# Optimization experiments

Hardware: AMD Instinct MI355X
Metric: run time of the kernel (lower is better)

## Reference

```python
import jax, jax.numpy as jnp
import numpy as np

L_F, HOP, DELTA, L_S, COND, GH = 32, 16, 3, 96, 32, 64
B, T = 128, 48000


def setup_inputs() -> dict:
    key = jax.random.key(0)
    ks = jax.random.split(key, 12)
    s = 0.05
    return {
        "x": jax.random.normal(ks[0], (B, T), jnp.float32),
        # GRU (PyTorch layout): weight_ih (3H, L_S), weight_hh (3H, H)
        "W_ih": jax.random.normal(ks[1], (3 * GH, L_S), jnp.float32) * s,
        "W_hh": jax.random.normal(ks[2], (3 * GH, GH), jnp.float32) * s,
        "b_ih": jax.random.normal(ks[3], (3 * GH,), jnp.float32) * s,
        "b_hh": jax.random.normal(ks[4], (3 * GH,), jnp.float32) * s,
        # SlowBranch output projection -> cond_dim
        "W_cs": jax.random.normal(ks[5], (COND, GH), jnp.float32) * s,
        "b_cs": jax.random.normal(ks[6], (COND,), jnp.float32) * s,
        # FastEC MLP
        "W1": jax.random.normal(ks[7], (GH, L_F + COND), jnp.float32) * s,
        "b1": jax.random.normal(ks[8], (GH,), jnp.float32) * s,
        "W2": jax.random.normal(ks[9], (L_F, GH), jnp.float32) * s,
        "b2": jax.random.normal(ks[10], (L_F,), jnp.float32) * s,
    }


def reference(x, W_ih, W_hh, b_ih, b_hh, W_cs, b_cs, W1, b1, W2, b2):
    Bsz, Tlen = x.shape
    Nf = (Tlen - L_F) // HOP + 1
    win_s = DELTA * HOP * 2
    hop_s = DELTA * HOP
    Ns = (Tlen - win_s) // hop_s + 1

    f_starts = jnp.arange(Nf) * HOP                      # (Nf,)
    fast_idx = f_starts[:, None] + jnp.arange(L_F)       # (Nf, L_F)
    fast_frames = x[:, fast_idx]                         # (B, Nf, L_F)

    s_starts = jnp.arange(Ns) * hop_s
    slow_frames = x[:, s_starts[:, None] + jnp.arange(win_s)]  # (B, Ns, L_S)

    # Single-layer GRU over slow frames (PyTorch gate order r, z, n)
    def step(h, xt):
        gi = xt @ W_ih.T + b_ih                          # (B, 3H)
        gh = h @ W_hh.T + b_hh
        i_r, i_z, i_n = jnp.split(gi, 3, axis=-1)
        h_r, h_z, h_n = jnp.split(gh, 3, axis=-1)
        r = jax.nn.sigmoid(i_r + h_r)
        z = jax.nn.sigmoid(i_z + h_z)
        n = jnp.tanh(i_n + r * h_n)
        hn = (1.0 - z) * n + z * h
        return hn, hn

    h0 = jnp.zeros((Bsz, GH), x.dtype)
    _, hs = jax.lax.scan(step, h0, jnp.swapaxes(slow_frames, 0, 1))
    hs = jnp.swapaxes(hs, 0, 1)                          # (B, Ns, GH)
    c_s = hs @ W_cs.T + b_cs                             # (B, Ns, COND)

    # per-fast-frame conditioning vector (gather)
    idx = jnp.clip(jnp.arange(Nf) // DELTA - 1, 0, None)
    c = c_s[:, idx]                                      # (B, Nf, COND)

    # FastEC batched over all frames at once
    h = jnp.concatenate([fast_frames, c], axis=-1)       # (B, Nf, L_F+COND)
    h = jax.nn.relu(h @ W1.T + b1)
    y = h @ W2.T + b2                                    # (B, Nf, L_F)

    # overlap-add scatter
    out = jnp.zeros_like(x).at[:, fast_idx].add(y)
    return out
```

## Files before the change

kernel.cpp:

```cpp
#include <hip/hip_runtime.h>

constexpr int Bn  = 128;
constexpr int Tn  = 48000;
constexpr int NFn = 2999;
constexpr int NSn = 999;
constexpr int G3n = 192;
constexpr int GHn = 64;

typedef float f2 __attribute__((ext_vector_type(2)));
typedef float f4 __attribute__((ext_vector_type(4)));

__global__ __launch_bounds__(192) void gi_kernel(const float* __restrict__ x,
                                                 const float* __restrict__ W_ih,
                                                 const float* __restrict__ b_ih,
                                                 float* __restrict__ GI) {
  __shared__ __align__(16) float WT[48 * 196];
  __shared__ __align__(16) float xs[1584];
  const int tile = blockIdx.x;
  const int b    = blockIdx.y;
  const int t0   = tile * 32;
  const int nt   = min(32, NSn - t0);
  const int tid  = threadIdx.x;

  const int span = (nt - 1) * 48 + 96;
  for (int i = tid; i < 1584; i += 192)
    xs[i] = (i < span) ? x[(size_t)b * Tn + t0 * 48 + i] : 0.0f;

  const int jq = tid % 48;
  const int tg = tid / 48;
  const int j0 = jq * 4;

  float acc[8][4];
#pragma unroll
  for (int u = 0; u < 8; ++u)
#pragma unroll
    for (int jj = 0; jj < 4; ++jj) acc[u][jj] = b_ih[j0 + jj];

  for (int half = 0; half < 2; ++half) {
    __syncthreads();
    for (int e = tid; e < 192 * 48; e += 192) {
      int j = e / 48, k = e % 48;
      WT[k * 196 + j] = W_ih[j * 96 + half * 48 + k];
    }
    __syncthreads();
    for (int kc = 0; kc < 48; kc += 4) {
      f4 wq[4];
#pragma unroll
      for (int kk = 0; kk < 4; ++kk)
        wq[kk] = *(const f4*)&WT[(kc + kk) * 196 + j0];
      f4 xq[8];
#pragma unroll
      for (int u = 0; u < 8; ++u)
        xq[u] = *(const f4*)&xs[(tg * 8 + u) * 48 + half * 48 + kc];
#pragma unroll
      for (int u = 0; u < 8; ++u) {
#pragma unroll
        for (int kk = 0; kk < 4; ++kk) {
          const float xv = xq[u][kk];
          acc[u][0] = fmaf(xv, wq[kk][0], acc[u][0]);
          acc[u][1] = fmaf(xv, wq[kk][1], acc[u][1]);
          acc[u][2] = fmaf(xv, wq[kk][2], acc[u][2]);
          acc[u][3] = fmaf(xv, wq[kk][3], acc[u][3]);
        }
      }
    }
  }

#pragma unroll
  for (int u = 0; u < 8; ++u) {
    int tl = tg * 8 + u;
    if (tl < nt) {
      float4 st = make_float4(acc[u][0], acc[u][1], acc[u][2], acc[u][3]);
      *(float4*)&GI[(size_t)(b * NSn + t0 + tl) * G3n + j0] = st;
    }
  }
}

__device__ __forceinline__ float fsigmoid(float v) {
  return __fdividef(1.0f, 1.0f + __expf(-v));
}
__device__ __forceinline__ float ftanh_f(float v) {
  return 1.0f - __fdividef(2.0f, __expf(2.0f * v) + 1.0f);
}

__device__ __forceinline__ void gru_body(const float* __restrict__ GI,
                                         const float* __restrict__ W_hh,
                                         const float* __restrict__ b_hh,
                                         float* __restrict__ hs,
                                         float* hbuf, int b, int j) {
  f2 wr2[32], wz2[32], wn2[32];
  const f2* Wr = (const f2*)(W_hh + (size_t)j * 64);
  const f2* Wz = (const f2*)(W_hh + (size_t)(j + 64) * 64);
  const f2* Wn = (const f2*)(W_hh + (size_t)(j + 128) * 64);
#pragma unroll
  for (int q = 0; q < 32; ++q) { wr2[q] = Wr[q]; wz2[q] = Wz[q]; wn2[q] = Wn[q]; }
#pragma unroll
  for (int q = 0; q < 32; ++q) {
    asm volatile("" : "+v"(wr2[q]));
    asm volatile("" : "+v"(wz2[q]));
    asm volatile("" : "+v"(wn2[q]));
  }
  const float br = b_hh[j], bz = b_hh[j + 64], bn = b_hh[j + 128];

  hbuf[j] = 0.0f;
  float hj = 0.0f;
  __builtin_amdgcn_wave_barrier();

  const float* gp = GI + (size_t)b * NSn * G3n;
  float* hsp = hs + (size_t)b * NSn * GHn;

  float pr0, pr1, pr2, pz0, pz1, pz2, pn0, pn1, pn2;
  pr0 = gp[0 * G3n + j];       pz0 = gp[0 * G3n + 64 + j];  pn0 = gp[0 * G3n + 128 + j];
  pr1 = gp[1 * G3n + j];       pz1 = gp[1 * G3n + 64 + j];  pn1 = gp[1 * G3n + 128 + j];

  for (int t = 0; t < NSn; ++t) {
    const size_t off = (size_t)min(t + 2, NSn - 1) * G3n;
    pr2 = gp[off + j];
    pz2 = gp[off + 64 + j];
    pn2 = gp[off + 128 + j];

    const f2* h2 = (const f2*)hbuf;
    f2 ar0 = {0.f, 0.f}, ar1 = {0.f, 0.f}, ar2 = {0.f, 0.f}, ar3 = {0.f, 0.f};
    f2 az0 = {0.f, 0.f}, az1 = {0.f, 0.f}, az2 = {0.f, 0.f}, az3 = {0.f, 0.f};
    f2 an0 = {0.f, 0.f}, an1 = {0.f, 0.f}, an2 = {0.f, 0.f}, an3 = {0.f, 0.f};
#pragma unroll
    for (int q = 0; q < 8; ++q) {
      f2 h0 = h2[q * 4 + 0], h1 = h2[q * 4 + 1], h2v = h2[q * 4 + 2], h3 = h2[q * 4 + 3];
      ar0 += wr2[q * 4 + 0] * h0; ar1 += wr2[q * 4 + 1] * h1;
      ar2 += wr2[q * 4 + 2] * h2v; ar3 += wr2[q * 4 + 3] * h3;
      az0 += wz2[q * 4 + 0] * h0; az1 += wz2[q * 4 + 1] * h1;
      az2 += wz2[q * 4 + 2] * h2v; az3 += wz2[q * 4 + 3] * h3;
      an0 += wn2[q * 4 + 0] * h0; an1 += wn2[q * 4 + 1] * h1;
      an2 += wn2[q * 4 + 2] * h2v; an3 += wn2[q * 4 + 3] * h3;
    }
    f2 sr = (ar0 + ar1) + (ar2 + ar3);
    f2 sz = (az0 + az1) + (az2 + az3);
    f2 sn = (an0 + an1) + (an2 + an3);

    float r = fsigmoid(pr0 + br + sr.x + sr.y);
    float z = fsigmoid(pz0 + bz + sz.x + sz.y);
    float n = ftanh_f(fmaf(r, bn + sn.x + sn.y, pn0));
    float hn = fmaf(z, hj - n, n);

    __builtin_amdgcn_wave_barrier();
    hbuf[j] = hn;
    __builtin_amdgcn_wave_barrier();
    hj = hn;
    hsp[(size_t)t * GHn + j] = hn;

    pr0 = pr1; pr1 = pr2;
    pz0 = pz1; pz1 = pz2;
    pn0 = pn1; pn1 = pn2;
  }
}

__global__ __attribute__((amdgpu_flat_work_group_size(64, 64),
                          amdgpu_waves_per_eu(1, 1),
                          amdgpu_num_vgpr(256)))
void gru_kernel(const float* __restrict__ GI,
                const float* __restrict__ W_hh,
                const float* __restrict__ b_hh,
                float* __restrict__ hs) {
  __shared__ __align__(16) float hbuf[64];
  gru_body(GI, W_hh, b_hh, hs, hbuf, blockIdx.x, threadIdx.x);
}

constexpr int UCHUNK = 125;
constexpr int NCH    = 24;

__global__ __attribute__((amdgpu_flat_work_group_size(64, 64),
                          amdgpu_waves_per_eu(1, 1),
                          amdgpu_num_vgpr(256)))
void fat_kernel(const float* __restrict__ GI,
                const float* __restrict__ W_hh,
                const float* __restrict__ b_hh,
                float* __restrict__ hs,
                const float* __restrict__ x,
                const float* __restrict__ W1,
                const float* __restrict__ b1,
                float* __restrict__ U) {
  __shared__ __align__(16) float hbuf[64];
  __shared__ __align__(16) float xs[UCHUNK * 16 + 16];
  const int tid = threadIdx.x;

  if (blockIdx.x < Bn) {
    __builtin_amdgcn_s_setprio(1);
    gru_body(GI, W_hh, b_hh, hs, hbuf, blockIdx.x, tid);
    __builtin_amdgcn_s_setprio(0);
    return;
  }

  const int ub = blockIdx.x - Bn;
  const int b  = ub / NCH;
  const int ch = ub % NCH;
  const int fA = ch * UCHUNK;
  const int fE = min(fA + UCHUNK, NFn);
  const int o  = tid;

  const int nsamp = (fE - fA - 1) * 16 + 32;
  for (int i = tid; i < nsamp; i += 64)
    xs[i] = x[(size_t)b * Tn + fA * 16 + i];

  f4 w1f[8];
#pragma unroll
  for (int i = 0; i < 8; ++i)
    w1f[i] = *(const f4*)&W1[(size_t)o * 64 + 4 * i];
  const float bo = b1[o];
  __syncthreads();

  float* Up = U + ((size_t)b * NFn) * GHn + o;
  for (int f = fA; f < fE; ++f) {
    const f4* xq = (const f4*)&xs[(f - fA) * 16];
    float a0 = bo, a1 = 0.f, a2 = 0.f, a3 = 0.f;
#pragma unroll
    for (int i = 0; i < 8; ++i) {
      f4 xv = xq[i];
      a0 = fmaf(xv[0], w1f[i][0], a0);
      a1 = fmaf(xv[1], w1f[i][1], a1);
      a2 = fmaf(xv[2], w1f[i][2], a2);
      a3 = fmaf(xv[3], w1f[i][3], a3);
    }
    Up[(size_t)f * GHn] = (a0 + a1) + (a2 + a3);
  }
}

__global__ __launch_bounds__(256) void d_kernel(const float* __restrict__ hs,
                                                const float* __restrict__ W_cs,
                                                const float* __restrict__ b_cs,
                                                const float* __restrict__ W1,
                                                float* __restrict__ d) {
  __shared__ __align__(16) float WcT[64 * 36];
  __shared__ __align__(16) float W1cT[32 * 68];
  __shared__ __align__(16) float hsl[32 * 65];
  __shared__ __align__(16) float cloc[32 * 36];
  __shared__ __align__(16) float bcs[32];
  const int tile = blockIdx.x;
  const int b    = blockIdx.y;
  const int t0   = tile * 32;
  const int nt   = min(32, NSn - t0);
  const int tid  = threadIdx.x;

  for (int e = tid; e < 32 * 64; e += 256) {
    int i = e >> 6, k = e & 63;
    WcT[k * 36 + i] = W_cs[e];
  }
  for (int e = tid; e < 64 * 32; e += 256) {
    int o = e >> 5, i = e & 31;
    W1cT[i * 68 + o] = W1[(size_t)o * 64 + 32 + i];
  }
  for (int e = tid; e < nt * 64; e += 256) {
    int t = e >> 6, k = e & 63;
    hsl[t * 65 + k] = hs[((size_t)b * NSn + t0 + t) * GHn + k];
  }
  if (tid < 32) bcs[tid] = b_cs[tid];
  __syncthreads();

  {
    const int iq = tid & 7;
    const int t  = tid >> 3;
    if (t < nt) {
      float4 acc = *(const float4*)&bcs[iq * 4];
      const float* hr = &hsl[t * 65];
#pragma unroll 4
      for (int k = 0; k < 64; ++k) {
        float hv = hr[k];
        float4 w = *(const float4*)&WcT[k * 36 + iq * 4];
        acc.x = fmaf(w.x, hv, acc.x);
        acc.y = fmaf(w.y, hv, acc.y);
        acc.z = fmaf(w.z, hv, acc.z);
        acc.w = fmaf(w.w, hv, acc.w);
      }
      *(float4*)&cloc[t * 36 + iq * 4] = acc;
    }
  }
  __syncthreads();

  for (int it = tid; it < 32 * 16; it += 256) {
    const int oq = it & 15;
    const int t  = it >> 4;
    if (t < nt) {
      float a0 = 0.f, a1 = 0.f, a2 = 0.f, a3 = 0.f;
      const float* cr = &cloc[t * 36];
#pragma unroll 4
      for (int i = 0; i < 32; ++i) {
        float cv = cr[i];
        float4 w = *(const float4*)&W1cT[i * 68 + oq * 4];
        a0 = fmaf(w.x, cv, a0);
        a1 = fmaf(w.y, cv, a1);
        a2 = fmaf(w.z, cv, a2);
        a3 = fmaf(w.w, cv, a3);
      }
      float4 st = make_float4(a0, a1, a2, a3);
      *(float4*)&d[((size_t)b * NSn + t0 + t) * GHn + oq * 4] = st;
    }
  }
}

__global__ __launch_bounds__(256) void cs_kernel(const float* __restrict__ hs,
                                                 const float* __restrict__ W_cs,
                                                 const float* __restrict__ b_cs,
                                                 float* __restrict__ cs) {
  __shared__ __align__(16) float WcT[64 * 36];
  __shared__ __align__(16) float hsl[32 * 65];
  __shared__ __align__(16) float bcs[32];
  const int tile = blockIdx.x;
  const int b    = blockIdx.y;
  const int t0   = tile * 32;
  const int nt   = min(32, NSn - t0);
  const int tid  = threadIdx.x;

  for (int e = tid; e < 32 * 64; e += 256) {
    int i = e >> 6, k = e & 63;
    WcT[k * 36 + i] = W_cs[e];
  }
  for (int e = tid; e < nt * 64; e += 256) {
    int t = e >> 6, k = e & 63;
    hsl[t * 65 + k] = hs[((size_t)b * NSn + t0 + t) * GHn + k];
  }
  if (tid < 32) bcs[tid] = b_cs[tid];
  __syncthreads();

  const int oq = tid & 7;
  const int t  = tid >> 3;
  if (t < nt) {
    float4 acc = *(const float4*)&bcs[oq * 4];
    const float* hr = &hsl[t * 65];
#pragma unroll 4
    for (int k = 0; k < 64; ++k) {
      float hv = hr[k];
      float4 w = *(const float4*)&WcT[k * 36 + oq * 4];
      acc.x = fmaf(w.x, hv, acc.x);
      acc.y = fmaf(w.y, hv, acc.y);
      acc.z = fmaf(w.z, hv, acc.z);
      acc.w = fmaf(w.w, hv, acc.w);
    }
    *(float4*)&cs[((size_t)b * NSn + t0 + t) * 32 + oq * 4] = acc;
  }
}

__global__ __launch_bounds__(256) void out2_kernel(const float* __restrict__ U,
                                                   const float* __restrict__ d,
                                                   const float* __restrict__ W2,
                                                   const float* __restrict__ b2,
                                                   float* __restrict__ out) {
  __shared__ __align__(16) float h1loc[33 * 68];
  __shared__ __align__(16) float W2T[64 * 36];
  __shared__ __align__(16) float yloc[33 * 32];
  __shared__ __align__(16) float dloc[12][68];
  __shared__ __align__(16) float bb2[32];

  const int fb  = blockIdx.x;
  const int b   = blockIdx.y;
  const int f0  = fb * 32;
  const int nf  = min(33, NFn - f0);
  const int tid = threadIdx.x;
  const int ts0 = max(f0 / 3 - 1, 0);

  for (int e = tid; e < 32 * 64; e += 256) {
    int o = e >> 6, k = e & 63;
    W2T[k * 36 + o] = W2[e];
  }
  if (tid < 32) bb2[tid] = b2[tid];
  for (int e = tid; e < 12 * 64; e += 256) {
    int ti = e >> 6, o = e & 63;
    int ts = min(ts0 + ti, NSn - 1);
    dloc[ti][o] = d[((size_t)b * NSn + ts) * GHn + o];
  }
  __syncthreads();

  for (int it = tid; it < 33 * 16; it += 256) {
    const int lf = it >> 4, oq = it & 15;
    const int f  = f0 + lf;
    f4 s = {0.f, 0.f, 0.f, 0.f};
    if (f < NFn) {
      f4 u  = *(const f4*)&U[((size_t)b * NFn + f) * GHn + oq * 4];
      const int ti = max(f / 3 - 1, 0) - ts0;
      f4 dv = *(const f4*)&dloc[ti][oq * 4];
      s = u + dv;
#pragma unroll
      for (int c = 0; c < 4; ++c) s[c] = fmaxf(s[c], 0.f);
    }
    *(f4*)&h1loc[lf * 68 + oq * 4] = s;
  }
  __syncthreads();

  for (int it = tid; it < 33 * 8; it += 256) {
    const int lf = it >> 3, oq = it & 7;
    float4 acc = *(const float4*)&bb2[oq * 4];
    const float* hr = &h1loc[lf * 68];
#pragma unroll 4
    for (int k = 0; k < 64; ++k) {
      float hv = hr[k];
      float4 w = *(const float4*)&W2T[k * 36 + oq * 4];
      acc.x = fmaf(w.x, hv, acc.x);
      acc.y = fmaf(w.y, hv, acc.y);
      acc.z = fmaf(w.z, hv, acc.z);
      acc.w = fmaf(w.w, hv, acc.w);
    }
    *(float4*)&yloc[lf * 32 + oq * 4] = acc;
  }
  __syncthreads();

  const int s0 = f0 * 16 + 16;
  const int s1 = min(s0 + 512, Tn);
  for (int s = s0 + tid; s < s1; s += 256) {
    int f1  = s >> 4;
    int o1  = s & 15;
    int lf1 = f1 - f0;
    float v = yloc[(lf1 - 1) * 32 + o1 + 16];
    if (lf1 < nf) v += yloc[lf1 * 32 + o1];
    out[(size_t)b * Tn + s] = v;
  }
  if (fb == 0 && tid < 16) out[(size_t)b * Tn + tid] = yloc[tid];
}

__global__ __launch_bounds__(256) void out_kernel(const float* __restrict__ x,
                                                  const float* __restrict__ cs,
                                                  const float* __restrict__ W1,
                                                  const float* __restrict__ b1,
                                                  const float* __restrict__ W2,
                                                  const float* __restrict__ b2,
                                                  float* __restrict__ out) {
  __shared__ __align__(16) float A[33 * 65];
  __shared__ __align__(16) float W1T[64 * 68];
  __shared__ __align__(16) float W2T[64 * 36];
  __shared__ __align__(16) float h1loc[33 * 65];
  __shared__ __align__(16) float yloc[33 * 32];
  __shared__ __align__(16) float bb1[64];
  __shared__ __align__(16) float bb2[32];

  const int fb  = blockIdx.x;
  const int b   = blockIdx.y;
  const int f0  = fb * 32;
  const int nf  = min(33, NFn - f0);
  const int tid = threadIdx.x;

  for (int e = tid; e < 64 * 64; e += 256) {
    int o = e >> 6, k = e & 63;
    W1T[k * 68 + o] = W1[e];
  }
  for (int e = tid; e < 32 * 64; e += 256) {
    int o = e >> 6, k = e & 63;
    W2T[k * 36 + o] = W2[e];
  }
  if (tid < 64) bb1[tid] = b1[tid];
  if (tid < 32) bb2[tid] = b2[tid];

  for (int e = tid; e < 33 * 32; e += 256) {
    int lf = e >> 5, k = e & 31;
    int g = (f0 + lf) * 16 + k;
    A[lf * 65 + k] = (lf < nf && g < Tn) ? x[(size_t)b * Tn + g] : 0.0f;
  }
  for (int e = tid; e < 33 * 32; e += 256) {
    int lf = e >> 5, k = e & 31;
    int ts = max((f0 + lf) / 3 - 1, 0);
    A[lf * 65 + 32 + k] = (lf < nf) ? cs[((size_t)b * NSn + ts) * 32 + k] : 0.0f;
  }
  __syncthreads();

  for (int it = tid; it < 33 * 16; it += 256) {
    int lf = it >> 4, oq = it & 15;
    float4 acc = *(const float4*)&bb1[oq * 4];
    const float* ar = &A[lf * 65];
#pragma unroll 4
    for (int k = 0; k < 64; ++k) {
      float av = ar[k];
      float4 w = *(const float4*)&W1T[k * 68 + oq * 4];
      acc.x = fmaf(w.x, av, acc.x);
      acc.y = fmaf(w.y, av, acc.y);
      acc.z = fmaf(w.z, av, acc.z);
      acc.w = fmaf(w.w, av, acc.w);
    }
    acc.x = fmaxf(acc.x, 0.0f); acc.y = fmaxf(acc.y, 0.0f);
    acc.z = fmaxf(acc.z, 0.0f); acc.w = fmaxf(acc.w, 0.0f);
    *(float4*)&h1loc[lf * 65 + oq * 4] = acc;
  }
  __syncthreads();

  for (int it = tid; it < 33 * 8; it += 256) {
    int lf = it >> 3, oq = it & 7;
    float4 acc = *(const float4*)&bb2[oq * 4];
    const float* hr = &h1loc[lf * 65];
#pragma unroll 4
    for (int k = 0; k < 64; ++k) {
      float hv = hr[k];
      float4 w = *(const float4*)&W2T[k * 36 + oq * 4];
      acc.x = fmaf(w.x, hv, acc.x);
      acc.y = fmaf(w.y, hv, acc.y);
      acc.z = fmaf(w.z, hv, acc.z);
      acc.w = fmaf(w.w, hv, acc.w);
    }
    *(float4*)&yloc[lf * 32 + oq * 4] = acc;
  }
  __syncthreads();

  const int s0 = f0 * 16 + 16;
  const int s1 = min(s0 + 512, Tn);
  for (int s = s0 + tid; s < s1; s += 256) {
    int f1  = s >> 4;
    int o1  = s & 15;
    int lf1 = f1 - f0;
    float v = yloc[(lf1 - 1) * 32 + o1 + 16];
    if (lf1 < nf) v += yloc[lf1 * 32 + o1];
    out[(size_t)b * Tn + s] = v;
  }
  if (fb == 0 && tid < 16) out[(size_t)b * Tn + tid] = yloc[tid];
}

extern "C" void kernel_launch(void* const* d_in, const int* in_sizes, int n_in,
                              void* d_out, int out_size, void* d_ws, size_t ws_size,
                              hipStream_t stream) {
  const float* x    = (const float*)d_in[0];
  const float* W_ih = (const float*)d_in[1];
  const float* W_hh = (const float*)d_in[2];
  const float* b_ih = (const float*)d_in[3];
  const float* b_hh = (const float*)d_in[4];
  const float* W_cs = (const float*)d_in[5];
  const float* b_cs = (const float*)d_in[6];
  const float* W1   = (const float*)d_in[7];
  const float* b1   = (const float*)d_in[8];
  const float* W2   = (const float*)d_in[9];
  const float* b2   = (const float*)d_in[10];
  float* out = (float*)d_out;

  const size_t giN = (size_t)Bn * NSn * G3n;
  const size_t hsN = (size_t)Bn * NSn * GHn;
  const size_t uN  = (size_t)Bn * NFn * GHn;

  float* GI = (float*)d_ws;
  float* hs = GI + giN;

  gi_kernel<<<dim3(32, Bn), 192, 0, stream>>>(x, W_ih, b_ih, GI);

  if (ws_size >= (giN + hsN + uN) * sizeof(float)) {
    float* U = hs + hsN;
    float* d = GI;
    fat_kernel<<<Bn + Bn * NCH, 64, 0, stream>>>(GI, W_hh, b_hh, hs,
                                                 x, W1, b1, U);
    d_kernel<<<dim3(32, Bn), 256, 0, stream>>>(hs, W_cs, b_cs, W1, d);
    out2_kernel<<<dim3(94, Bn), 256, 0, stream>>>(U, d, W2, b2, out);
  } else {
    float* cs = GI;
    gru_kernel<<<Bn, 64, 0, stream>>>(GI, W_hh, b_hh, hs);
    cs_kernel<<<dim3(32, Bn), 256, 0, stream>>>(hs, W_cs, b_cs, cs);
    out_kernel<<<dim3(94, Bn), 256, 0, stream>>>(x, cs, W1, b1, W2, b2, out);
  }
}
```

Measured before the change: 768.0 us.

## Fuse GI projection into GRU block via double-buffered LDS producer-consumer ring

Replaces the separate gi_kernel plus fat_kernel with one fused kernel. In each GRU block, two producer waves compute the input projection for the next 32 timesteps into a double-buffered LDS ring while wave 0 runs the recurrence, so the GI tensor no longer goes through global memory. The U-precompute blocks are repacked as three waves per block. This drops one launch and the GI global write/read, but the 192-thread GRU blocks with 128KB LDS reduce occupancy, and a block barrier per chunk may stall the serial recurrence if production is slower.

Result: slower. 951.9 us (+24.0%).

```diff
diff --git a/kernel.cpp b/kernel.cpp
--- a/kernel.cpp
+++ b/kernel.cpp
@@ -10,50 +10,51 @@
 typedef float f2 __attribute__((ext_vector_type(2)));
 typedef float f4 __attribute__((ext_vector_type(4)));
 
-__global__ __launch_bounds__(192) void gi_kernel(const float* __restrict__ x,
-                                                 const float* __restrict__ W_ih,
-                                                 const float* __restrict__ b_ih,
-                                                 float* __restrict__ GI) {
-  __shared__ __align__(16) float WT[48 * 196];
-  __shared__ __align__(16) float xs[1584];
-  const int tile = blockIdx.x;
-  const int b    = blockIdx.y;
-  const int t0   = tile * 32;
-  const int nt   = min(32, NSn - t0);
-  const int tid  = threadIdx.x;
-
+#define LBAR()                                                 \
+  do {                                                         \
+    asm volatile("s_waitcnt lgkmcnt(0)" ::: "memory");         \
+    __builtin_amdgcn_s_barrier();                              \
+    asm volatile("" ::: "memory");                             \
+  } while (0)
+
+__device__ __forceinline__ float fsigmoid(float v) {
+  return __fdividef(1.0f, 1.0f + __expf(-v));
+}
+__device__ __forceinline__ float ftanh_f(float v) {
+  return 1.0f - __fdividef(2.0f, __expf(2.0f * v) + 1.0f);
+}
+
+__device__ __forceinline__ void produce_chunk(const float* __restrict__ x,
+                                              int b, int c,
+                                              float* __restrict__ ring_slot,
+                                              float* __restrict__ xs,
+                                              const float* __restrict__ WT,
+                                              int tg2, int lane, f4 bias4) {
+  const int nt   = min(32, NSn - c * 32);
   const int span = (nt - 1) * 48 + 96;
-  for (int i = tid; i < 1584; i += 192)
-    xs[i] = (i < span) ? x[(size_t)b * Tn + t0 * 48 + i] : 0.0f;
-
-  const int jq = tid % 48;
-  const int tg = tid / 48;
-  const int j0 = jq * 4;
-
-  float acc[8][4];
-#pragma unroll
-  for (int u = 0; u < 8; ++u)
-#pragma unroll
-    for (int jj = 0; jj < 4; ++jj) acc[u][jj] = b_ih[j0 + jj];
-
-  for (int half = 0; half < 2; ++half) {
-    __syncthreads();
-    for (int e = tid; e < 192 * 48; e += 192) {
-      int j = e / 48, k = e % 48;
-      WT[k * 196 + j] = W_ih[j * 96 + half * 48 + k];
-    }
-    __syncthreads();
-    for (int kc = 0; kc < 48; kc += 4) {
+  for (int i = lane; i < 816; i += 64) {
+    const int ii = tg2 * 768 + i;
+    xs[ii] = (ii < span) ? x[(size_t)b * Tn + (size_t)c * 1536 + ii] : 0.0f;
+  }
+  __builtin_amdgcn_wave_barrier();
+  asm volatile("s_waitcnt lgkmcnt(0)" ::: "memory");
+
+  if (lane < 48) {
+    const int j0 = lane * 4;
+    f4 acc[16];
+#pragma unroll
+    for (int u = 0; u < 16; ++u) acc[u] = bias4;
+    for (int kc = 0; kc < 96; kc += 4) {
       f4 wq[4];
 #pragma unroll
       for (int kk = 0; kk < 4; ++kk)
         wq[kk] = *(const f4*)&WT[(kc + kk) * 196 + j0];
-      f4 xq[8];
-#pragma unroll
-      for (int u = 0; u < 8; ++u)
-        xq[u] = *(const f4*)&xs[(tg * 8 + u) * 48 + half * 48 + kc];
-#pragma unroll
-      for (int u = 0; u < 8; ++u) {
+      f4 xq[16];
+#pragma unroll
+      for (int u = 0; u < 16; ++u)
+        xq[u] = *(const f4*)&xs[(tg2 * 16 + u) * 48 + kc];
+#pragma unroll
+      for (int u = 0; u < 16; ++u) {
 #pragma unroll
         for (int kk = 0; kk < 4; ++kk) {
           const float xv = xq[u][kk];
@@ -64,163 +65,158 @@
         }
       }
     }
-  }
-
-#pragma unroll
-  for (int u = 0; u < 8; ++u) {
-    int tl = tg * 8 + u;
-    if (tl < nt) {
-      float4 st = make_float4(acc[u][0], acc[u][1], acc[u][2], acc[u][3]);
-      *(float4*)&GI[(size_t)(b * NSn + t0 + tl) * G3n + j0] = st;
-    }
-  }
-}
-
-__device__ __forceinline__ float fsigmoid(float v) {
-  return __fdividef(1.0f, 1.0f + __expf(-v));
-}
-__device__ __forceinline__ float ftanh_f(float v) {
-  return 1.0f - __fdividef(2.0f, __expf(2.0f * v) + 1.0f);
-}
-
-__device__ __forceinline__ void gru_body(const float* __restrict__ GI,
-                                         const float* __restrict__ W_hh,
-                                         const float* __restrict__ b_hh,
-                                         float* __restrict__ hs,
-                                         float* hbuf, int b, int j) {
-  f2 wr2[32], wz2[32], wn2[32];
-  const f2* Wr = (const f2*)(W_hh + (size_t)j * 64);
-  const f2* Wz = (const f2*)(W_hh + (size_t)(j + 64) * 64);
-  const f2* Wn = (const f2*)(W_hh + (size_t)(j + 128) * 64);
-#pragma unroll
-  for (int q = 0; q < 32; ++q) { wr2[q] = Wr[q]; wz2[q] = Wz[q]; wn2[q] = Wn[q]; }
-#pragma unroll
-  for (int q = 0; q < 32; ++q) {
-    asm volatile("" : "+v"(wr2[q]));
-    asm volatile("" : "+v"(wz2[q]));
-    asm volatile("" : "+v"(wn2[q]));
-  }
-  const float br = b_hh[j], bz = b_hh[j + 64], bn = b_hh[j + 128];
-
-  hbuf[j] = 0.0f;
-  float hj = 0.0f;
-  __builtin_amdgcn_wave_barrier();
-
-  const float* gp = GI + (size_t)b * NSn * G3n;
-  float* hsp = hs + (size_t)b * NSn * GHn;
-
-  float pr0, pr1, pr2, pz0, pz1, pz2, pn0, pn1, pn2;
-  pr0 = gp[0 * G3n + j];       pz0 = gp[0 * G3n + 64 + j];  pn0 = gp[0 * G3n + 128 + j];
-  pr1 = gp[1 * G3n + j];       pz1 = gp[1 * G3n + 64 + j];  pn1 = gp[1 * G3n + 128 + j];
-
-  for (int t = 0; t < NSn; ++t) {
-    const size_t off = (size_t)min(t + 2, NSn - 1) * G3n;
-    pr2 = gp[off + j];
-    pz2 = gp[off + 64 + j];
-    pn2 = gp[off + 128 + j];
-
-    const f2* h2 = (const f2*)hbuf;
-    f2 ar0 = {0.f, 0.f}, ar1 = {0.f, 0.f}, ar2 = {0.f, 0.f}, ar3 = {0.f, 0.f};
-    f2 az0 = {0.f, 0.f}, az1 = {0.f, 0.f}, az2 = {0.f, 0.f}, az3 = {0.f, 0.f};
-    f2 an0 = {0.f, 0.f}, an1 = {0.f, 0.f}, an2 = {0.f, 0.f}, an3 = {0.f, 0.f};
-#pragma unroll
-    for (int q = 0; q < 8; ++q) {
-      f2 h0 = h2[q * 4 + 0], h1 = h2[q * 4 + 1], h2v = h2[q * 4 + 2], h3 = h2[q * 4 + 3];
-      ar0 += wr2[q * 4 + 0] * h0; ar1 += wr2[q * 4 + 1] * h1;
-      ar2 += wr2[q * 4 + 2] * h2v; ar3 += wr2[q * 4 + 3] * h3;
-      az0 += wz2[q * 4 + 0] * h0; az1 += wz2[q * 4 + 1] * h1;
-      az2 += wz2[q * 4 + 2] * h2v; az3 += wz2[q * 4 + 3] * h3;
-      an0 += wn2[q * 4 + 0] * h0; an1 += wn2[q * 4 + 1] * h1;
-      an2 += wn2[q * 4 + 2] * h2v; an3 += wn2[q * 4 + 3] * h3;
-    }
-    f2 sr = (ar0 + ar1) + (ar2 + ar3);
-    f2 sz = (az0 + az1) + (az2 + az3);
-    f2 sn = (an0 + an1) + (an2 + an3);
-
-    float r = fsigmoid(pr0 + br + sr.x + sr.y);
-    float z = fsigmoid(pz0 + bz + sz.x + sz.y);
-    float n = ftanh_f(fmaf(r, bn + sn.x + sn.y, pn0));
-    float hn = fmaf(z, hj - n, n);
-
-    __builtin_amdgcn_wave_barrier();
-    hbuf[j] = hn;
-    __builtin_amdgcn_wave_barrier();
-    hj = hn;
-    hsp[(size_t)t * GHn + j] = hn;
-
-    pr0 = pr1; pr1 = pr2;
-    pz0 = pz1; pz1 = pz2;
-    pn0 = pn1; pn1 = pn2;
-  }
-}
-
-__global__ __attribute__((amdgpu_flat_work_group_size(64, 64),
+#pragma unroll
+    for (int u = 0; u < 16; ++u) {
+      const int tl = tg2 * 16 + u;
+      if (tl < nt) *(f4*)&ring_slot[tl * 192 + j0] = acc[u];
+    }
+  }
+}
+
+constexpr int UCHUNK = 125;
+
+__global__ __attribute__((amdgpu_flat_work_group_size(192, 192),
                           amdgpu_waves_per_eu(1, 1),
                           amdgpu_num_vgpr(256)))
-void gru_kernel(const float* __restrict__ GI,
-                const float* __restrict__ W_hh,
-                const float* __restrict__ b_hh,
-                float* __restrict__ hs) {
-  __shared__ __align__(16) float hbuf[64];
-  gru_body(GI, W_hh, b_hh, hs, hbuf, blockIdx.x, threadIdx.x);
-}
-
-constexpr int UCHUNK = 125;
-constexpr int NCH    = 24;
-
-__global__ __attribute__((amdgpu_flat_work_group_size(64, 64),
-                          amdgpu_waves_per_eu(1, 1),
-                          amdgpu_num_vgpr(256)))
-void fat_kernel(const float* __restrict__ GI,
-                const float* __restrict__ W_hh,
-                const float* __restrict__ b_hh,
-                float* __restrict__ hs,
-                const float* __restrict__ x,
-                const float* __restrict__ W1,
-                const float* __restrict__ b1,
-                float* __restrict__ U) {
-  __shared__ __align__(16) float hbuf[64];
-  __shared__ __align__(16) float xs[UCHUNK * 16 + 16];
-  const int tid = threadIdx.x;
-
-  if (blockIdx.x < Bn) {
-    __builtin_amdgcn_s_setprio(1);
-    gru_body(GI, W_hh, b_hh, hs, hbuf, blockIdx.x, tid);
-    __builtin_amdgcn_s_setprio(0);
+void fused_kernel(const float* __restrict__ x,
+                  const float* __restrict__ W_ih,
+                  const float* __restrict__ b_ih,
+                  const float* __restrict__ W_hh,
+                  const float* __restrict__ b_hh,
+                  const float* __restrict__ W1,
+                  const float* __restrict__ b1,
+                  float* __restrict__ hs,
+                  float* __restrict__ U) {
+  __shared__ __align__(16) float smem[32752];
+  const int tid  = threadIdx.x;
+  const int wid  = tid >> 6;
+  const int lane = tid & 63;
+
+  if (blockIdx.x >= Bn) {
+    const int ub = blockIdx.x - Bn;
+    const int b  = ub >> 3;
+    const int ch = (ub & 7) * 3 + wid;
+    const int fA = ch * UCHUNK;
+    const int fE = min(fA + UCHUNK, NFn);
+    float* xu = smem + wid * 2016;
+    const int nsamp = (fE - fA - 1) * 16 + 32;
+    for (int i = lane; i < nsamp; i += 64)
+      xu[i] = x[(size_t)b * Tn + fA * 16 + i];
+    f4 w1f[8];
+#pragma unroll
+    for (int i = 0; i < 8; ++i)
+      w1f[i] = *(const f4*)&W1[(size_t)lane * 64 + 4 * i];
+    const float bo = b1[lane];
+    __builtin_amdgcn_wave_barrier();
+    asm volatile("s_waitcnt lgkmcnt(0)" ::: "memory");
+
+    float* Up = U + ((size_t)b * NFn) * GHn + lane;
+    for (int f = fA; f < fE; ++f) {
+      const f4* xq2 = (const f4*)&xu[(f - fA) * 16];
+      float a0 = bo, a1 = 0.f, a2 = 0.f, a3 = 0.f;
+#pragma unroll
+      for (int i = 0; i < 8; ++i) {
+        f4 xv = xq2[i];
+        a0 = fmaf(xv[0], w1f[i][0], a0);
+        a1 = fmaf(xv[1], w1f[i][1], a1);
+        a2 = fmaf(xv[2], w1f[i][2], a2);
+        a3 = fmaf(xv[3], w1f[i][3], a3);
+      }
+      Up[(size_t)f * GHn] = (a0 + a1) + (a2 + a3);
+    }
     return;
   }
 
-  const int ub = blockIdx.x - Bn;
-  const int b  = ub / NCH;
-  const int ch = ub % NCH;
-  const int fA = ch * UCHUNK;
-  const int fE = min(fA + UCHUNK, NFn);
-  const int o  = tid;
-
-  const int nsamp = (fE - fA - 1) * 16 + 32;
-  for (int i = tid; i < nsamp; i += 64)
-    xs[i] = x[(size_t)b * Tn + fA * 16 + i];
-
-  f4 w1f[8];
-#pragma unroll
-  for (int i = 0; i < 8; ++i)
-    w1f[i] = *(const f4*)&W1[(size_t)o * 64 + 4 * i];
-  const float bo = b1[o];
-  __syncthreads();
-
-  float* Up = U + ((size_t)b * NFn) * GHn + o;
-  for (int f = fA; f < fE; ++f) {
-    const f4* xq = (const f4*)&xs[(f - fA) * 16];
-    float a0 = bo, a1 = 0.f, a2 = 0.f, a3 = 0.f;
-#pragma unroll
-    for (int i = 0; i < 8; ++i) {
-      f4 xv = xq[i];
-      a0 = fmaf(xv[0], w1f[i][0], a0);
-      a1 = fmaf(xv[1], w1f[i][1], a1);
-      a2 = fmaf(xv[2], w1f[i][2], a2);
-      a3 = fmaf(xv[3], w1f[i][3], a3);
-    }
-    Up[(size_t)f * GHn] = (a0 + a1) + (a2 + a3);
+  const int b = blockIdx.x;
+  float* WT   = smem;
+  float* ring = smem + 18816;
+  float* xs   = smem + 31104;
+  float* hbuf = smem + 32688;
+
+  for (int e4 = tid * 4; e4 < 192 * 96; e4 += 192 * 4) {
+    f4 v = *(const f4*)&W_ih[e4];
+    const int j = e4 / 96, k = e4 - j * 96;
+#pragma unroll
+    for (int cc = 0; cc < 4; ++cc) WT[(k + cc) * 196 + j] = v[cc];
+  }
+  LBAR();
+
+  f2 wr2[32], wz2[32], wn2[32];
+  float br = 0.f, bz = 0.f, bn = 0.f;
+  f4 bias4 = {0.f, 0.f, 0.f, 0.f};
+  const int tg2 = wid - 1;
+
+  if (wid == 0) {
+    const int j = lane;
+    const f2* Wr = (const f2*)(W_hh + (size_t)j * 64);
+    const f2* Wz = (const f2*)(W_hh + (size_t)(j + 64) * 64);
+    const f2* Wn = (const f2*)(W_hh + (size_t)(j + 128) * 64);
+#pragma unroll
+    for (int q = 0; q < 32; ++q) { wr2[q] = Wr[q]; wz2[q] = Wz[q]; wn2[q] = Wn[q]; }
+#pragma unroll
+    for (int q = 0; q < 32; ++q) {
+      asm volatile("" : "+v"(wr2[q]));
+      asm volatile("" : "+v"(wz2[q]));
+      asm volatile("" : "+v"(wn2[q]));
+    }
+    br = b_hh[j]; bz = b_hh[j + 64]; bn = b_hh[j + 128];
+    hbuf[j] = 0.0f;
+  } else {
+    if (lane < 48) bias4 = *(const f4*)&b_ih[lane * 4];
+    produce_chunk(x, b, 0, ring, xs, WT, tg2, lane, bias4);
+  }
+  LBAR();
+
+  float hj = 0.0f;
+  float* hsp = hs + (size_t)b * NSn * GHn;
+
+  for (int p = 0; p < 32; ++p) {
+    if (wid == 0) {
+      __builtin_amdgcn_s_setprio(1);
+      const int j  = lane;
+      const int nt = min(32, NSn - p * 32);
+      const float* rs = ring + (p & 1) * 6144;
+      for (int tt = 0; tt < nt; ++tt) {
+        const float* grow = rs + tt * 192;
+        const float pr0 = grow[j];
+        const float pz0 = grow[64 + j];
+        const float pn0 = grow[128 + j];
+
+        const f2* h2 = (const f2*)hbuf;
+        f2 ar0 = {0.f, 0.f}, ar1 = {0.f, 0.f}, ar2 = {0.f, 0.f}, ar3 = {0.f, 0.f};
+        f2 az0 = {0.f, 0.f}, az1 = {0.f, 0.f}, az2 = {0.f, 0.f}, az3 = {0.f, 0.f};
+        f2 an0 = {0.f, 0.f}, an1 = {0.f, 0.f}, an2 = {0.f, 0.f}, an3 = {0.f, 0.f};
+#pragma unroll
+        for (int q = 0; q < 8; ++q) {
+          f2 h0 = h2[q * 4 + 0], h1 = h2[q * 4 + 1], h2v = h2[q * 4 + 2], h3 = h2[q * 4 + 3];
+          ar0 += wr2[q * 4 + 0] * h0; ar1 += wr2[q * 4 + 1] * h1;
+          ar2 += wr2[q * 4 + 2] * h2v; ar3 += wr2[q * 4 + 3] * h3;
+          az0 += wz2[q * 4 + 0] * h0; az1 += wz2[q * 4 + 1] * h1;
+          az2 += wz2[q * 4 + 2] * h2v; az3 += wz2[q * 4 + 3] * h3;
+          an0 += wn2[q * 4 + 0] * h0; an1 += wn2[q * 4 + 1] * h1;
+          an2 += wn2[q * 4 + 2] * h2v; an3 += wn2[q * 4 + 3] * h3;
+        }
+        f2 sr = (ar0 + ar1) + (ar2 + ar3);
+        f2 sz = (az0 + az1) + (az2 + az3);
+        f2 sn = (an0 + an1) + (an2 + an3);
+
+        float r = fsigmoid(pr0 + br + sr.x + sr.y);
+        float z = fsigmoid(pz0 + bz + sz.x + sz.y);
+        float n = ftanh_f(fmaf(r, bn + sn.x + sn.y, pn0));
+        float hn = fmaf(z, hj - n, n);
+
+        __builtin_amdgcn_wave_barrier();
+        hbuf[j] = hn;
+        __builtin_amdgcn_wave_barrier();
+        hj = hn;
+        hsp[(size_t)(p * 32 + tt) * GHn + j] = hn;
+      }
+      __builtin_amdgcn_s_setprio(0);
+    } else if (p + 1 < 32) {
+      produce_chunk(x, b, p + 1, ring + ((p + 1) & 1) * 6144, xs, WT,
+                    tg2, lane, bias4);
+    }
+    LBAR();
   }
 }
 
@@ -296,6 +292,215 @@
   }
 }
 
+__global__ __launch_bounds__(256) void out2_kernel(const float* __restrict__ U,
+                                                   const float* __restrict__ d,
+                                                   const float* __restrict__ W2,
+                                                   const float* __restrict__ b2,
+                                                   float* __restrict__ out) {
+  __shared__ __align__(16) float h1loc[33 * 68];
+  __shared__ __align__(16) float W2T[64 * 36];
+  __shared__ __align__(16) float yloc[33 * 32];
+  __shared__ __align__(16) float dloc[12][68];
+  __shared__ __align__(16) float bb2[32];
+
+  const int fb  = blockIdx.x;
+  const int b   = blockIdx.y;
+  const int f0  = fb * 32;
+  const int nf  = min(33, NFn - f0);
+  const int tid = threadIdx.x;
+  const int ts0 = max(f0 / 3 - 1, 0);
+
+  for (int e = tid; e < 32 * 64; e += 256) {
+    int o = e >> 6, k = e & 63;
+    W2T[k * 36 + o] = W2[e];
+  }
+  if (tid < 32) bb2[tid] = b2[tid];
+  for (int e = tid; e < 12 * 64; e += 256) {
+    int ti = e >> 6, o = e & 63;
+    int ts = min(ts0 + ti, NSn - 1);
+    dloc[ti][o] = d[((size_t)b * NSn + ts) * GHn + o];
+  }
+  __syncthreads();
+
+  for (int it = tid; it < 33 * 16; it += 256) {
+    const int lf = it >> 4, oq = it & 15;
+    const int f  = f0 + lf;
+    f4 s = {0.f, 0.f, 0.f, 0.f};
+    if (f < NFn) {
+      f4 u  = *(const f4*)&U[((size_t)b * NFn + f) * GHn + oq * 4];
+      const int ti = max(f / 3 - 1, 0) - ts0;
+      f4 dv = *(const f4*)&dloc[ti][oq * 4];
+      s = u + dv;
+#pragma unroll
+      for (int c = 0; c < 4; ++c) s[c] = fmaxf(s[c], 0.f);
+    }
+    *(f4*)&h1loc[lf * 68 + oq * 4] = s;
+  }
+  __syncthreads();
+
+  for (int it = tid; it < 33 * 8; it += 256) {
+    const int lf = it >> 3, oq = it & 7;
+    float4 acc = *(const float4*)&bb2[oq * 4];
+    const float* hr = &h1loc[lf * 68];
+#pragma unroll 4
+    for (int k = 0; k < 64; ++k) {
+      float hv = hr[k];
+      float4 w = *(const float4*)&W2T[k * 36 + oq * 4];
+      acc.x = fmaf(w.x, hv, acc.x);
+      acc.y = fmaf(w.y, hv, acc.y);
+      acc.z = fmaf(w.z, hv, acc.z);
+      acc.w = fmaf(w.w, hv, acc.w);
+    }
+    *(float4*)&yloc[lf * 32 + oq * 4] = acc;
+  }
+  __syncthreads();
+
+  const int s0 = f0 * 16 + 16;
+  const int s1 = min(s0 + 512, Tn);
+  for (int s = s0 + tid; s < s1; s += 256) {
+    int f1  = s >> 4;
+    int o1  = s & 15;
+    int lf1 = f1 - f0;
+    float v = yloc[(lf1 - 1) * 32 + o1 + 16];
+    if (lf1 < nf) v += yloc[lf1 * 32 + o1];
+    out[(size_t)b * Tn + s] = v;
+  }
+  if (fb == 0 && tid < 16) out[(size_t)b * Tn + tid] = yloc[tid];
+}
+
+__global__ __launch_bounds__(192) void gi_kernel(const float* __restrict__ x,
+                                                 const float* __restrict__ W_ih,
+                                                 const float* __restrict__ b_ih,
+                                                 float* __restrict__ GI) {
+  __shared__ __align__(16) float WT[48 * 196];
+  __shared__ __align__(16) float xs[1584];
+  const int tile = blockIdx.x;
+  const int b    = blockIdx.y;
+  const int t0   = tile * 32;
+  const int nt   = min(32, NSn - t0);
+  const int tid  = threadIdx.x;
+
+  const int span = (nt - 1) * 48 + 96;
+  for (int i = tid; i < 1584; i += 192)
+    xs[i] = (i < span) ? x[(size_t)b * Tn + t0 * 48 + i] : 0.0f;
+
+  const int jq = tid % 48;
+  const int tg = tid / 48;
+  const int j0 = jq * 4;
+
+  float acc[8][4];
+#pragma unroll
+  for (int u = 0; u < 8; ++u)
+#pragma unroll
+    for (int jj = 0; jj < 4; ++jj) acc[u][jj] = b_ih[j0 + jj];
+
+  for (int half = 0; half < 2; ++half) {
+    __syncthreads();
+    for (int e = tid; e < 192 * 48; e += 192) {
+      int j = e / 48, k = e % 48;
+      WT[k * 196 + j] = W_ih[j * 96 + half * 48 + k];
+    }
+    __syncthreads();
+    for (int k = 0; k < 48; ++k) {
+      float4 w = *(const float4*)&WT[k * 196 + j0];
+#pragma unroll
+      for (int u = 0; u < 8; ++u) {
+        float xv = xs[(tg * 8 + u) * 48 + half * 48 + k];
+        acc[u][0] = fmaf(xv, w.x, acc[u][0]);
+        acc[u][1] = fmaf(xv, w.y, acc[u][1]);
+        acc[u][2] = fmaf(xv, w.z, acc[u][2]);
+        acc[u][3] = fmaf(xv, w.w, acc[u][3]);
+      }
+    }
+  }
+
+#pragma unroll
+  for (int u = 0; u < 8; ++u) {
+    int tl = tg * 8 + u;
+    if (tl < nt) {
+      float4 st = make_float4(acc[u][0], acc[u][1], acc[u][2], acc[u][3]);
+      *(float4*)&GI[(size_t)(b * NSn + t0 + tl) * G3n + j0] = st;
+    }
+  }
+}
+
+__global__ __attribute__((amdgpu_flat_work_group_size(64, 64),
+                          amdgpu_waves_per_eu(1, 1),
+                          amdgpu_num_vgpr(256)))
+void gru_kernel(const float* __restrict__ GI,
+                const float* __restrict__ W_hh,
+                const float* __restrict__ b_hh,
+                float* __restrict__ hs) {
+  __shared__ __align__(16) float hbuf[64];
+  const int b = blockIdx.x;
+  const int j = threadIdx.x;
+
+  f2 wr2[32], wz2[32], wn2[32];
+  const f2* Wr = (const f2*)(W_hh + (size_t)j * 64);
+  const f2* Wz = (const f2*)(W_hh + (size_t)(j + 64) * 64);
+  const f2* Wn = (const f2*)(W_hh + (size_t)(j + 128) * 64);
+#pragma unroll
+  for (int q = 0; q < 32; ++q) { wr2[q] = Wr[q]; wz2[q] = Wz[q]; wn2[q] = Wn[q]; }
+#pragma unroll
+  for (int q = 0; q < 32; ++q) {
+    asm volatile("" : "+v"(wr2[q]));
+    asm volatile("" : "+v"(wz2[q]));
+    asm volatile("" : "+v"(wn2[q]));
+  }
+  const float br = b_hh[j], bz = b_hh[j + 64], bn = b_hh[j + 128];
+
+  hbuf[j] = 0.0f;
+  float hj = 0.0f;
+  __builtin_amdgcn_wave_barrier();
+
+  const float* gp = GI + (size_t)b * NSn * G3n;
+  float* hsp = hs + (size_t)b * NSn * GHn;
+
+  float pr0, pr1, pr2, pz0, pz1, pz2, pn0, pn1, pn2;
+  pr0 = gp[0 * G3n + j];       pz0 = gp[0 * G3n + 64 + j];  pn0 = gp[0 * G3n + 128 + j];
+  pr1 = gp[1 * G3n + j];       pz1 = gp[1 * G3n + 64 + j];  pn1 = gp[1 * G3n + 128 + j];
+
+  for (int t = 0; t < NSn; ++t) {
+    const size_t off = (size_t)min(t + 2, NSn - 1) * G3n;
+    pr2 = gp[off + j];
+    pz2 = gp[off + 64 + j];
+    pn2 = gp[off + 128 + j];
+
+    const f2* h2 = (const f2*)hbuf;
+    f2 ar0 = {0.f, 0.f}, ar1 = {0.f, 0.f}, ar2 = {0.f, 0.f}, ar3 = {0.f, 0.f};
+    f2 az0 = {0.f, 0.f}, az1 = {0.f, 0.f}, az2 = {0.f, 0.f}, az3 = {0.f, 0.f};
+    f2 an0 = {0.f, 0.f}, an1 = {0.f, 0.f}, an2 = {0.f, 0.f}, an3 = {0.f, 0.f};
+#pragma unroll
+    for (int q = 0; q < 8; ++q) {
+      f2 h0 = h2[q * 4 + 0], h1 = h2[q * 4 + 1], h2v = h2[q * 4 + 2], h3 = h2[q * 4 + 3];
+      ar0 += wr2[q * 4 + 0] * h0; ar1 += wr2[q * 4 + 1] * h1;
+      ar2 += wr2[q * 4 + 2] * h2v; ar3 += wr2[q * 4 + 3] * h3;
+      az0 += wz2[q * 4 + 0] * h0; az1 += wz2[q * 4 + 1] * h1;
+      az2 += wz2[q * 4 + 2] * h2v; az3 += wz2[q * 4 + 3] * h3;
+      an0 += wn2[q * 4 + 0] * h0; an1 += wn2[q * 4 + 1] * h1;
+      an2 += wn2[q * 4 + 2] * h2v; an3 += wn2[q * 4 + 3] * h3;
+    }
+    f2 sr = (ar0 + ar1) + (ar2 + ar3);
+    f2 sz = (az0 + az1) + (az2 + az3);
+    f2 sn = (an0 + an1) + (an2 + an3);
+
+    float r = fsigmoid(pr0 + br + sr.x + sr.y);
+    float z = fsigmoid(pz0 + bz + sz.x + sz.y);
+    float n = ftanh_f(fmaf(r, bn + sn.x + sn.y, pn0));
+    float hn = fmaf(z, hj - n, n);
+
+    __builtin_amdgcn_wave_barrier();
+    hbuf[j] = hn;
+    __builtin_amdgcn_wave_barrier();
+    hj = hn;
+    hsp[(size_t)t * GHn + j] = hn;
+
+    pr0 = pr1; pr1 = pr2;
+    pz0 = pz1; pz1 = pz2;
+    pn0 = pn1; pn1 = pn2;
+  }
+}
+
 __global__ __launch_bounds__(256) void cs_kernel(const float* __restrict__ hs,
                                                  const float* __restrict__ W_cs,
                                                  const float* __restrict__ b_cs,
@@ -336,82 +541,6 @@
     }
     *(float4*)&cs[((size_t)b * NSn + t0 + t) * 32 + oq * 4] = acc;
   }
-}
-
-__global__ __launch_bounds__(256) void out2_kernel(const float* __restrict__ U,
-                                                   const float* __restrict__ d,
-                                                   const float* __restrict__ W2,
-                                                   const float* __restrict__ b2,
-                                                   float* __restrict__ out) {
-  __shared__ __align__(16) float h1loc[33 * 68];
-  __shared__ __align__(16) float W2T[64 * 36];
-  __shared__ __align__(16) float yloc[33 * 32];
-  __shared__ __align__(16) float dloc[12][68];
-  __shared__ __align__(16) float bb2[32];
-
-  const int fb  = blockIdx.x;
-  const int b   = blockIdx.y;
-  const int f0  = fb * 32;
-  const int nf  = min(33, NFn - f0);
-  const int tid = threadIdx.x;
-  const int ts0 = max(f0 / 3 - 1, 0);
-
-  for (int e = tid; e < 32 * 64; e += 256) {
-    int o = e >> 6, k = e & 63;
-    W2T[k * 36 + o] = W2[e];
-  }
-  if (tid < 32) bb2[tid] = b2[tid];
-  for (int e = tid; e < 12 * 64; e += 256) {
-    int ti = e >> 6, o = e & 63;
-    int ts = min(ts0 + ti, NSn - 1);
-    dloc[ti][o] = d[((size_t)b * NSn + ts) * GHn + o];
-  }
-  __syncthreads();
-
-  for (int it = tid; it < 33 * 16; it += 256) {
-    const int lf = it >> 4, oq = it & 15;
-    const int f  = f0 + lf;
-    f4 s = {0.f, 0.f, 0.f, 0.f};
-    if (f < NFn) {
-      f4 u  = *(const f4*)&U[((size_t)b * NFn + f) * GHn + oq * 4];
-      const int ti = max(f / 3 - 1, 0) - ts0;
-      f4 dv = *(const f4*)&dloc[ti][oq * 4];
-      s = u + dv;
-#pragma unroll
-      for (int c = 0; c < 4; ++c) s[c] = fmaxf(s[c], 0.f);
-    }
-    *(f4*)&h1loc[lf * 68 + oq * 4] = s;
-  }
-  __syncthreads();
-
-  for (int it = tid; it < 33 * 8; it += 256) {
-    const int lf = it >> 3, oq = it & 7;
-    float4 acc = *(const float4*)&bb2[oq * 4];
-    const float* hr = &h1loc[lf * 68];
-#pragma unroll 4
-    for (int k = 0; k < 64; ++k) {
-      float hv = hr[k];
-      float4 w = *(const float4*)&W2T[k * 36 + oq * 4];
-      acc.x = fmaf(w.x, hv, acc.x);
-      acc.y = fmaf(w.y, hv, acc.y);
-      acc.z = fmaf(w.z, hv, acc.z);
-      acc.w = fmaf(w.w, hv, acc.w);
-    }
-    *(float4*)&yloc[lf * 32 + oq * 4] = acc;
-  }
-  __syncthreads();
-
-  const int s0 = f0 * 16 + 16;
-  const int s1 = min(s0 + 512, Tn);
-  for (int s = s0 + tid; s < s1; s += 256) {
-    int f1  = s >> 4;
-    int o1  = s & 15;
-    int lf1 = f1 - f0;
-    float v = yloc[(lf1 - 1) * 32 + o1 + 16];
-    if (lf1 < nf) v += yloc[lf1 * 32 + o1];
-    out[(size_t)b * Tn + s] = v;
-  }
-  if (fb == 0 && tid < 16) out[(size_t)b * Tn + tid] = yloc[tid];
 }
 
 __global__ __launch_bounds__(256) void out_kernel(const float* __restrict__ x,
@@ -523,24 +652,24 @@
   const float* b2   = (const float*)d_in[10];
   float* out = (float*)d_out;
 
-  const size_t giN = (size_t)Bn * NSn * G3n;
   const size_t hsN = (size_t)Bn * NSn * GHn;
   const size_t uN  = (size_t)Bn * NFn * GHn;
-
-  float* GI = (float*)d_ws;
-  float* hs = GI + giN;
-
-  gi_kernel<<<dim3(32, Bn), 192, 0, stream>>>(x, W_ih, b_ih, GI);
-
-  if (ws_size >= (giN + hsN + uN) * sizeof(float)) {
-    float* U = hs + hsN;
-    float* d = GI;
-    fat_kernel<<<Bn + Bn * NCH, 64, 0, stream>>>(GI, W_hh, b_hh, hs,
-                                                 x, W1, b1, U);
+  const size_t dN  = hsN;
+  const size_t giN = (size_t)Bn * NSn * G3n;
+
+  if (ws_size >= (hsN + uN + dN) * sizeof(float)) {
+    float* hs = (float*)d_ws;
+    float* U  = hs + hsN;
+    float* d  = U + uN;
+    fused_kernel<<<Bn + Bn * 8, 192, 0, stream>>>(x, W_ih, b_ih, W_hh, b_hh,
+                                                  W1, b1, hs, U);
     d_kernel<<<dim3(32, Bn), 256, 0, stream>>>(hs, W_cs, b_cs, W1, d);
     out2_kernel<<<dim3(94, Bn), 256, 0, stream>>>(U, d, W2, b2, out);
   } else {
+    float* GI = (float*)d_ws;
+    float* hs = GI + giN;
     float* cs = GI;
+    gi_kernel<<<dim3(32, Bn), 192, 0, stream>>>(x, W_ih, b_ih, GI);
     gru_kernel<<<Bn, 64, 0, stream>>>(GI, W_hh, b_hh, hs);
     cs_kernel<<<dim3(32, Bn), 256, 0, stream>>>(hs, W_cs, b_cs, cs);
     out_kernel<<<dim3(94, Bn), 256, 0, stream>>>(x, cs, W1, b1, W2, b2, out);
```
